# Performance work log

Hardware: AMD Instinct MI355X
Metric: run time of the kernel (lower is better)

Reference implementation:

```python
import jax, jax.numpy as jnp
import numpy as np

GRID_SIZE = 5
SPLINE_ORDER = 3
GRID_RANGE = (-1.0, 1.0)
BN_EPS = 1e-5


def _make_grid():
    h = (GRID_RANGE[1] - GRID_RANGE[0]) / GRID_SIZE
    # grid_size + 2*spline_order + 1 = 12 knots, shared across the 9 patch features
    return jnp.arange(-SPLINE_ORDER, GRID_SIZE + SPLINE_ORDER + 1, dtype=jnp.float32) * h + GRID_RANGE[0]


def _b_splines(x, grid):
    # x: (N, F) -> (N, F, grid_size + spline_order) via Cox-de Boor recursion
    x = x[..., None]
    bases = ((x >= grid[:-1]) & (x < grid[1:])).astype(x.dtype)
    for k in range(1, SPLINE_ORDER + 1):
        left = (x - grid[: -(k + 1)]) / (grid[k:-1] - grid[: -(k + 1)]) * bases[..., :-1]
        right = (grid[k + 1:] - x) / (grid[k + 1:] - grid[1:-k]) * bases[..., 1:]
        bases = left + right
    return bases


def setup_inputs() -> dict:
    key = jax.random.key(0)
    ks = jax.random.split(key, 4)
    B, C, H, W = 4, 64, 96, 96
    return {
        "x": jax.random.normal(ks[0], (B, C, H, W), dtype=jnp.float32),
        "base_weight": jax.random.normal(ks[1], (1, 9), dtype=jnp.float32) * 0.3,
        "spline_weight": jax.random.normal(ks[2], (1, 9, GRID_SIZE + SPLINE_ORDER), dtype=jnp.float32) * 0.3,
        "spline_scaler": jax.random.normal(ks[3], (1, 9), dtype=jnp.float32) * 0.3 + 1.0,
        "bn_gamma": jnp.ones((C,), dtype=jnp.float32),
        "bn_beta": jnp.zeros((C,), dtype=jnp.float32),
    }


def reference(x, base_weight, spline_weight, spline_scaler, bn_gamma, bn_beta):
    B, C, H, W = x.shape
    grid = _make_grid()
    # Per-channel depthwise 3x3 patch extraction (pad 1, stride 1), shared KANLinear(9 -> 1)
    patches = jax.lax.conv_general_dilated_patches(
        x.reshape(B * C, 1, H, W), (3, 3), (1, 1), [(1, 1), (1, 1)]
    )  # (B*C, 9, H, W)
    tok = patches.transpose(0, 2, 3, 1).reshape(-1, 9)  # (N, 9)

    base_out = jax.nn.silu(tok) @ base_weight.T  # (N, 1)
    bases = _b_splines(tok, grid)  # (N, 9, 8)
    scaled_sw = (spline_weight * spline_scaler[..., None]).reshape(1, -1)  # (1, 72)
    spline_out = bases.reshape(tok.shape[0], -1) @ scaled_sw.T  # (N, 1)

    y = (base_out + spline_out).reshape(B, C, H, W)

    # BatchNorm2d (training-mode batch statistics) + ReLU
    mean = y.mean(axis=(0, 2, 3))
    var = y.var(axis=(0, 2, 3))
    y_hat = (y - mean[None, :, None, None]) * jax.lax.rsqrt(var + BN_EPS)[None, :, None, None]
    out = jax.nn.relu(y_hat * bn_gamma[None, :, None, None] + bn_beta[None, :, None, None])
    return out
```

## Files before the change

### kernel.cpp

```cpp
#include <hip/hip_runtime.h>
#include <math.h>

#define HH 96
#define WW 96
#define CC 64
#define BB 4
#define PLANE (HH * WW)
#define NPLANES (BB * CC)
#define NPC (BB * PLANE)
#define TILE 32
#define TPL 3
#define NTILES (TPL * TPL)
#define HALO 34
#define HALO_N (HALO * HALO)
#define BLOCK 256

typedef _Float16 h2v __attribute__((ext_vector_type(2)));

static __device__ __forceinline__ float dot2h(unsigned a, unsigned b, float c) {
#if __has_builtin(__builtin_amdgcn_fdot2)
    return __builtin_amdgcn_fdot2(__builtin_bit_cast(h2v, a),
                                  __builtin_bit_cast(h2v, b), c, false);
#else
    h2v x = __builtin_bit_cast(h2v, a);
    h2v y = __builtin_bit_cast(h2v, b);
    return c + (float)x[0] * (float)y[0] + (float)x[1] * (float)y[1];
#endif
}

static __device__ __forceinline__ unsigned pk16(float a, float b) {
    return __builtin_bit_cast(unsigned, __builtin_amdgcn_cvt_pkrtz(a, b));
}


__global__ __launch_bounds__(BLOCK) void kconv_stage1(
    const float* __restrict__ x,
    const float* __restrict__ base_w,
    const float* __restrict__ spline_w,
    const float* __restrict__ spline_s,
    float* __restrict__ y,
    float2* __restrict__ part)
{
    __shared__ uint4  s_n[HALO_N];
    __shared__ float  s_sl[HALO_N];
    __shared__ unsigned s_wp[36];
    __shared__ float  s_bw[9];
    __shared__ float2 red[4];

    const int tid = threadIdx.x;

    if (tid < 36) {
        const int j = tid >> 2;
        const int k = tid & 3;
        const float sc = spline_s[j];
        s_wp[tid] = pk16(spline_w[j * 8 + 2 * k] * sc,
                         spline_w[j * 8 + 2 * k + 1] * sc);
    }
    if (tid < 9) s_bw[tid] = base_w[tid];

    const int plane = blockIdx.y;
    const int h0 = blockIdx.x * TILE;
    const float* xp = x + (size_t)plane * PLANE;

    int hy[5], hx[5];
#pragma unroll
    for (int s = 0; s < 5; ++s) {
        const int i = tid + s * BLOCK;
        const int r = i / HALO;
        hy[s] = r;
        hx[s] = i - r * HALO;
    }

    const int tx  = tid & 31;
    const int ty4 = (tid >> 5) * 4;

    for (int wt = 0; wt < TPL; ++wt) {
        const int w0 = wt * TILE;

        float v[5];
#pragma unroll
        for (int s = 0; s < 5; ++s) {
            const int gh = h0 + hy[s] - 1;
            const int gw = w0 + hx[s] - 1;
            const bool ok = (tid + s * BLOCK < HALO_N) &&
                            gh >= 0 && gh < HH && gw >= 0 && gw < WW;
            v[s] = ok ? xp[gh * WW + gw] : 0.0f;
        }

        if (wt == 0) __syncthreads();

#pragma unroll
        for (int s = 0; s < 5; ++s) {
            const int i = tid + s * BLOCK;
            if (i >= HALO_N) break;
            const float vv = v[s];
            const float e  = __expf(-vv);
            const float sl = vv * __builtin_amdgcn_rcpf(1.0f + e);

            const float sp = fmaf(vv, 2.5f, 2.5f);
            const float tf = floorf(sp);
            const float u  = sp - tf;
            const int   t  = (int)tf;
            const int   m  = t >> 1;
            const bool  odd = (t & 1) != 0;

            const float w1m = 1.0f - u;
            const float u2 = u * u;
            const float u3 = u2 * u;
            const float B0 = w1m * w1m * (w1m * (1.0f / 6.0f));
            const float B3 = u2 * (u * (1.0f / 6.0f));
            const float B1 = fmaf(-u2, 1.0f, fmaf(u3, 0.5f, 2.0f / 3.0f));
            const float B2 = 1.0f - B0 - B1 - B3;

            const unsigned h01 = pk16(B0, B1);
            const unsigned h23 = pk16(B2, B3);

            unsigned n[4];
            unsigned a_prev;
            {
                const int k0 = -1 - m;
                a_prev = (k0 == 0) ? h01 : ((k0 == 1) ? h23 : 0u);
            }
#pragma unroll
            for (int d = 0; d < 4; ++d) {
                const int k0 = d - m;
                const unsigned a_cur = (k0 == 0) ? h01 : ((k0 == 1) ? h23 : 0u);
                const unsigned sh = __builtin_amdgcn_alignbit(a_cur, a_prev, 16);
                n[d] = odd ? sh : a_cur;
                a_prev = a_cur;
            }
            s_n[i]  = make_uint4(n[0], n[1], n[2], n[3]);
            s_sl[i] = sl;
        }
        __syncthreads();

        unsigned wp[36];
        float bw[9];
#pragma unroll
        for (int q = 0; q < 36; ++q)
            wp[q] = __builtin_amdgcn_readfirstlane(s_wp[q]);
#pragma unroll
        for (int q = 0; q < 9; ++q)
            bw[q] = __int_as_float(__builtin_amdgcn_readfirstlane(__float_as_int(s_bw[q])));

        float acc[4] = {0.0f, 0.0f, 0.0f, 0.0f};
#pragma unroll
        for (int r = 0; r < 6; ++r) {
            const int base = (ty4 + r) * HALO + tx;
            uint4 cn[3];
            float cs[3];
#pragma unroll
            for (int dw = 0; dw < 3; ++dw) {
                cn[dw] = s_n[base + dw];
                cs[dw] = s_sl[base + dw];
            }
#pragma unroll
            for (int k = 0; k < 4; ++k) {
                const int dh = r - k;
                if (dh >= 0 && dh < 3) {
#pragma unroll
                    for (int dw = 0; dw < 3; ++dw) {
                        const int j = dh * 3 + dw;
                        float a = acc[k];
                        a = dot2h(cn[dw].x, wp[j * 4 + 0], a);
                        a = dot2h(cn[dw].y, wp[j * 4 + 1], a);
                        a = dot2h(cn[dw].z, wp[j * 4 + 2], a);
                        a = dot2h(cn[dw].w, wp[j * 4 + 3], a);
                        a = fmaf(bw[j], cs[dw], a);
                        acc[k] = a;
                    }
                }
            }
        }

        float lsum = 0.0f, lsq = 0.0f;
        float* yp = y + (size_t)plane * PLANE + (size_t)h0 * WW + w0;
#pragma unroll
        for (int k = 0; k < 4; ++k) {
            yp[(ty4 + k) * WW + tx] = acc[k];
            lsum += acc[k];
            lsq = fmaf(acc[k], acc[k], lsq);
        }

#pragma unroll
        for (int off = 32; off; off >>= 1) {
            lsum += __shfl_down(lsum, off, 64);
            lsq  += __shfl_down(lsq,  off, 64);
        }
        if ((tid & 63) == 0) red[tid >> 6] = make_float2(lsum, lsq);
        __syncthreads();
        if (tid == 0) {
            const float s = red[0].x + red[1].x + red[2].x + red[3].x;
            const float q = red[0].y + red[1].y + red[2].y + red[3].y;
            part[plane * NTILES + blockIdx.x * TPL + wt] = make_float2(s, q);
        }
    }
}

__global__ __launch_bounds__(BLOCK) void kconv_stage2(
    float* __restrict__ y,
    const float2* __restrict__ part,
    const float* __restrict__ gamma,
    const float* __restrict__ beta)
{
    __shared__ float2 sb;
    const int tid = threadIdx.x;
    const int plane = blockIdx.x;
    const int c = plane & (CC - 1);

    if (tid < 64) {
        float s = 0.0f, q = 0.0f;
        if (tid < 36) {
            const int b = tid / 9;
            const int t = tid - b * 9;
            const float2 pp = part[(c + CC * b) * NTILES + t];
            s = pp.x; q = pp.y;
        }
#pragma unroll
        for (int off = 32; off; off >>= 1) {
            s += __shfl_down(s, off, 64);
            q += __shfl_down(q, off, 64);
        }
        if (tid == 0) {
            const float inv = 1.0f / (float)NPC;
            const float mean = s * inv;
            const float var  = q * inv - mean * mean;
            const float sc   = rsqrtf(var + 1e-5f) * gamma[c];
            sb = make_float2(sc, beta[c] - mean * sc);
        }
    }
    __syncthreads();
    const float2 sbv = sb;

    float4* yp = (float4*)(y + (size_t)plane * PLANE + (size_t)blockIdx.y * 1024);
    float4 v = yp[tid];
    v.x = fmaxf(fmaf(v.x, sbv.x, sbv.y), 0.0f);
    v.y = fmaxf(fmaf(v.y, sbv.x, sbv.y), 0.0f);
    v.z = fmaxf(fmaf(v.z, sbv.x, sbv.y), 0.0f);
    v.w = fmaxf(fmaf(v.w, sbv.x, sbv.y), 0.0f);
    yp[tid] = v;
}

extern "C" void kernel_launch(void* const* d_in, const int* in_sizes, int n_in,
                              void* d_out, int out_size, void* d_ws, size_t ws_size,
                              hipStream_t stream)
{
    const float* x        = (const float*)d_in[0];
    const float* base_w   = (const float*)d_in[1];
    const float* spline_w = (const float*)d_in[2];
    const float* spline_s = (const float*)d_in[3];
    const float* gamma    = (const float*)d_in[4];
    const float* beta     = (const float*)d_in[5];
    float* out   = (float*)d_out;
    float2* part = (float2*)d_ws;

    dim3 g1(TPL, NPLANES);
    kconv_stage1<<<g1, BLOCK, 0, stream>>>(x, base_w, spline_w, spline_s, out, part);

    dim3 g2(NPLANES, PLANE / (BLOCK * 4));
    kconv_stage2<<<g2, BLOCK, 0, stream>>>(out, part, gamma, beta);
}
```

Measured before the change: 86.23 us.

## Use 16-row strips per block with deferred stores and single stats reduction

Stage 1 now gives each block a 16x96 strip instead of a 32x96 band, so the grid doubles to 6 strips per plane and each thread computes 2 rows per tile instead of 4. Accumulators for all three column tiles are kept in registers and written out at the end, with one block reduction and one partial-stat write per strip. Weight broadcast is hoisted out of the tile loop and launch bounds request 6 blocks per SM. This raises parallelism and cuts per-tile syncs, but increases halo recomputation (18 rows per 16 outputs versus 34 per 32) and register pressure.

```diff
diff --git a/kernel.cpp b/kernel.cpp
--- a/kernel.cpp
+++ b/kernel.cpp
@@ -8,11 +8,13 @@
 #define PLANE (HH * WW)
 #define NPLANES (BB * CC)
 #define NPC (BB * PLANE)
-#define TILE 32
+#define TILE_W 32
+#define TILE_H 16
+#define STRIPS (HH / TILE_H)
 #define TPL 3
-#define NTILES (TPL * TPL)
-#define HALO 34
-#define HALO_N (HALO * HALO)
+#define HALO_W 34
+#define HALO_H 18
+#define HALO_N (HALO_H * HALO_W)
 #define BLOCK 256
 
 typedef _Float16 h2v __attribute__((ext_vector_type(2)));
@@ -33,7 +35,7 @@
 }
 
 
-__global__ __launch_bounds__(BLOCK) void kconv_stage1(
+__global__ __launch_bounds__(BLOCK, 6) void kconv_stage1(
     const float* __restrict__ x,
     const float* __restrict__ base_w,
     const float* __restrict__ spline_w,
@@ -59,27 +61,42 @@
     if (tid < 9) s_bw[tid] = base_w[tid];
 
     const int plane = blockIdx.y;
-    const int h0 = blockIdx.x * TILE;
+    const int strip = blockIdx.x;
+    const int h0 = strip * TILE_H;
     const float* xp = x + (size_t)plane * PLANE;
 
-    int hy[5], hx[5];
-#pragma unroll
-    for (int s = 0; s < 5; ++s) {
+    int hy[3], hx[3];
+#pragma unroll
+    for (int s = 0; s < 3; ++s) {
         const int i = tid + s * BLOCK;
-        const int r = i / HALO;
+        const int r = i / HALO_W;
         hy[s] = r;
-        hx[s] = i - r * HALO;
+        hx[s] = i - r * HALO_W;
     }
 
     const int tx  = tid & 31;
-    const int ty4 = (tid >> 5) * 4;
-
+    const int ty2 = (tid >> 5) * 2;
+
+    __syncthreads();
+
+    unsigned wp[36];
+    float bw[9];
+#pragma unroll
+    for (int q = 0; q < 36; ++q)
+        wp[q] = __builtin_amdgcn_readfirstlane(s_wp[q]);
+#pragma unroll
+    for (int q = 0; q < 9; ++q)
+        bw[q] = __int_as_float(__builtin_amdgcn_readfirstlane(__float_as_int(s_bw[q])));
+
+    float acc[TPL][2] = {};
+
+#pragma unroll
     for (int wt = 0; wt < TPL; ++wt) {
-        const int w0 = wt * TILE;
-
-        float v[5];
-#pragma unroll
-        for (int s = 0; s < 5; ++s) {
+        const int w0 = wt * TILE_W;
+
+        float v[3];
+#pragma unroll
+        for (int s = 0; s < 3; ++s) {
             const int gh = h0 + hy[s] - 1;
             const int gw = w0 + hx[s] - 1;
             const bool ok = (tid + s * BLOCK < HALO_N) &&
@@ -87,10 +104,10 @@
             v[s] = ok ? xp[gh * WW + gw] : 0.0f;
         }
 
-        if (wt == 0) __syncthreads();
-
-#pragma unroll
-        for (int s = 0; s < 5; ++s) {
+        if (wt) __syncthreads();
+
+#pragma unroll
+        for (int s = 0; s < 3; ++s) {
             const int i = tid + s * BLOCK;
             if (i >= HALO_N) break;
             const float vv = v[s];
@@ -134,19 +151,9 @@
         }
         __syncthreads();
 
-        unsigned wp[36];
-        float bw[9];
-#pragma unroll
-        for (int q = 0; q < 36; ++q)
-            wp[q] = __builtin_amdgcn_readfirstlane(s_wp[q]);
-#pragma unroll
-        for (int q = 0; q < 9; ++q)
-            bw[q] = __int_as_float(__builtin_amdgcn_readfirstlane(__float_as_int(s_bw[q])));
-
-        float acc[4] = {0.0f, 0.0f, 0.0f, 0.0f};
-#pragma unroll
-        for (int r = 0; r < 6; ++r) {
-            const int base = (ty4 + r) * HALO + tx;
+#pragma unroll
+        for (int r = 0; r < 4; ++r) {
+            const int base = (ty2 + r) * HALO_W + tx;
             uint4 cn[3];
             float cs[3];
 #pragma unroll
@@ -155,45 +162,49 @@
                 cs[dw] = s_sl[base + dw];
             }
 #pragma unroll
-            for (int k = 0; k < 4; ++k) {
+            for (int k = 0; k < 2; ++k) {
                 const int dh = r - k;
                 if (dh >= 0 && dh < 3) {
+                    float a = acc[wt][k];
 #pragma unroll
                     for (int dw = 0; dw < 3; ++dw) {
                         const int j = dh * 3 + dw;
-                        float a = acc[k];
                         a = dot2h(cn[dw].x, wp[j * 4 + 0], a);
                         a = dot2h(cn[dw].y, wp[j * 4 + 1], a);
                         a = dot2h(cn[dw].z, wp[j * 4 + 2], a);
                         a = dot2h(cn[dw].w, wp[j * 4 + 3], a);
                         a = fmaf(bw[j], cs[dw], a);
-                        acc[k] = a;
                     }
+                    acc[wt][k] = a;
                 }
             }
         }
-
-        float lsum = 0.0f, lsq = 0.0f;
-        float* yp = y + (size_t)plane * PLANE + (size_t)h0 * WW + w0;
-#pragma unroll
-        for (int k = 0; k < 4; ++k) {
-            yp[(ty4 + k) * WW + tx] = acc[k];
-            lsum += acc[k];
-            lsq = fmaf(acc[k], acc[k], lsq);
-        }
-
-#pragma unroll
-        for (int off = 32; off; off >>= 1) {
-            lsum += __shfl_down(lsum, off, 64);
-            lsq  += __shfl_down(lsq,  off, 64);
-        }
-        if ((tid & 63) == 0) red[tid >> 6] = make_float2(lsum, lsq);
-        __syncthreads();
-        if (tid == 0) {
-            const float s = red[0].x + red[1].x + red[2].x + red[3].x;
-            const float q = red[0].y + red[1].y + red[2].y + red[3].y;
-            part[plane * NTILES + blockIdx.x * TPL + wt] = make_float2(s, q);
-        }
+    }
+
+    float lsum = 0.0f, lsq = 0.0f;
+    float* ypl = y + (size_t)plane * PLANE + (size_t)h0 * WW;
+#pragma unroll
+    for (int wt = 0; wt < TPL; ++wt) {
+#pragma unroll
+        for (int k = 0; k < 2; ++k) {
+            const float a = acc[wt][k];
+            ypl[(ty2 + k) * WW + wt * TILE_W + tx] = a;
+            lsum += a;
+            lsq = fmaf(a, a, lsq);
+        }
+    }
+
+#pragma unroll
+    for (int off = 32; off; off >>= 1) {
+        lsum += __shfl_down(lsum, off, 64);
+        lsq  += __shfl_down(lsq,  off, 64);
+    }
+    if ((tid & 63) == 0) red[tid >> 6] = make_float2(lsum, lsq);
+    __syncthreads();
+    if (tid == 0) {
+        const float s = red[0].x + red[1].x + red[2].x + red[3].x;
+        const float q = red[0].y + red[1].y + red[2].y + red[3].y;
+        part[plane * STRIPS + strip] = make_float2(s, q);
     }
 }
 
@@ -210,10 +221,10 @@
 
     if (tid < 64) {
         float s = 0.0f, q = 0.0f;
-        if (tid < 36) {
-            const int b = tid / 9;
-            const int t = tid - b * 9;
-            const float2 pp = part[(c + CC * b) * NTILES + t];
+        if (tid < BB * STRIPS) {
+            const int b = tid / STRIPS;
+            const int t = tid - b * STRIPS;
+            const float2 pp = part[(c + CC * b) * STRIPS + t];
             s = pp.x; q = pp.y;
         }
 #pragma unroll
@@ -254,7 +265,7 @@
     float* out   = (float*)d_out;
     float2* part = (float2*)d_ws;
 
-    dim3 g1(TPL, NPLANES);
+    dim3 g1(STRIPS, NPLANES);
     kconv_stage1<<<g1, BLOCK, 0, stream>>>(x, base_w, spline_w, spline_s, out, part);
 
     dim3 g2(NPLANES, PLANE / (BLOCK * 4));
```

Result: slower. 127.9 us (+48.3%).

## Fuse BatchNorm into conv kernel via cooperative grid sync, keeping outputs in registers

Applied to the files above, without the earlier changes.

Makes each block hold accumulators for all three width tiles in registers, and reduces the per-block partial sums to one (sum, sumsq) pair per block. The kernel launches cooperatively, synchronizes the whole grid, then applies BN and ReLU directly from registers. This drops the second kernel launch and the global write/read round trip of y. The cost is higher register pressure and a grid-wide barrier over 768 blocks that must all be resident at once. If the cooperative launch fails, it falls back to the two-kernel path.

```diff
diff --git a/kernel.cpp b/kernel.cpp
--- a/kernel.cpp
+++ b/kernel.cpp
@@ -1,5 +1,8 @@
 #include <hip/hip_runtime.h>
+#include <hip/hip_cooperative_groups.h>
 #include <math.h>
+
+namespace cg = cooperative_groups;
 
 #define HH 96
 #define WW 96
@@ -10,7 +13,6 @@
 #define NPC (BB * PLANE)
 #define TILE 32
 #define TPL 3
-#define NTILES (TPL * TPL)
 #define HALO 34
 #define HALO_N (HALO * HALO)
 #define BLOCK 256
@@ -33,11 +35,14 @@
 }
 
 
-__global__ __launch_bounds__(BLOCK) void kconv_stage1(
+template <int COOP>
+__global__ __launch_bounds__(BLOCK) void kconv_main(
     const float* __restrict__ x,
     const float* __restrict__ base_w,
     const float* __restrict__ spline_w,
     const float* __restrict__ spline_s,
+    const float* __restrict__ gamma,
+    const float* __restrict__ beta,
     float* __restrict__ y,
     float2* __restrict__ part)
 {
@@ -46,6 +51,7 @@
     __shared__ unsigned s_wp[36];
     __shared__ float  s_bw[9];
     __shared__ float2 red[4];
+    __shared__ float2 sb;
 
     const int tid = threadIdx.x;
 
@@ -59,6 +65,8 @@
     if (tid < 9) s_bw[tid] = base_w[tid];
 
     const int plane = blockIdx.y;
+    const int c = plane & (CC - 1);
+    const int b = plane >> 6;
     const int h0 = blockIdx.x * TILE;
     const float* xp = x + (size_t)plane * PLANE;
 
@@ -73,6 +81,11 @@
 
     const int tx  = tid & 31;
     const int ty4 = (tid >> 5) * 4;
+
+    float acc[TPL][4] = {};
+
+    unsigned wp[36];
+    float bw[9];
 
     for (int wt = 0; wt < TPL; ++wt) {
         const int w0 = wt * TILE;
@@ -87,7 +100,16 @@
             v[s] = ok ? xp[gh * WW + gw] : 0.0f;
         }
 
-        if (wt == 0) __syncthreads();
+        __syncthreads();
+
+        if (wt == 0) {
+#pragma unroll
+            for (int q = 0; q < 36; ++q)
+                wp[q] = __builtin_amdgcn_readfirstlane(s_wp[q]);
+#pragma unroll
+            for (int q = 0; q < 9; ++q)
+                bw[q] = __int_as_float(__builtin_amdgcn_readfirstlane(__float_as_int(s_bw[q])));
+        }
 
 #pragma unroll
         for (int s = 0; s < 5; ++s) {
@@ -134,16 +156,6 @@
         }
         __syncthreads();
 
-        unsigned wp[36];
-        float bw[9];
-#pragma unroll
-        for (int q = 0; q < 36; ++q)
-            wp[q] = __builtin_amdgcn_readfirstlane(s_wp[q]);
-#pragma unroll
-        for (int q = 0; q < 9; ++q)
-            bw[q] = __int_as_float(__builtin_amdgcn_readfirstlane(__float_as_int(s_bw[q])));
-
-        float acc[4] = {0.0f, 0.0f, 0.0f, 0.0f};
 #pragma unroll
         for (int r = 0; r < 6; ++r) {
             const int base = (ty4 + r) * HALO + tx;
@@ -158,46 +170,87 @@
             for (int k = 0; k < 4; ++k) {
                 const int dh = r - k;
                 if (dh >= 0 && dh < 3) {
+                    float a = acc[wt][k];
 #pragma unroll
                     for (int dw = 0; dw < 3; ++dw) {
                         const int j = dh * 3 + dw;
-                        float a = acc[k];
                         a = dot2h(cn[dw].x, wp[j * 4 + 0], a);
                         a = dot2h(cn[dw].y, wp[j * 4 + 1], a);
                         a = dot2h(cn[dw].z, wp[j * 4 + 2], a);
                         a = dot2h(cn[dw].w, wp[j * 4 + 3], a);
                         a = fmaf(bw[j], cs[dw], a);
-                        acc[k] = a;
                     }
+                    acc[wt][k] = a;
                 }
             }
         }
-
-        float lsum = 0.0f, lsq = 0.0f;
-        float* yp = y + (size_t)plane * PLANE + (size_t)h0 * WW + w0;
+    }
+
+    float lsum = 0.0f, lsq = 0.0f;
+#pragma unroll
+    for (int wt = 0; wt < TPL; ++wt)
 #pragma unroll
         for (int k = 0; k < 4; ++k) {
-            yp[(ty4 + k) * WW + tx] = acc[k];
-            lsum += acc[k];
-            lsq = fmaf(acc[k], acc[k], lsq);
-        }
-
-#pragma unroll
-        for (int off = 32; off; off >>= 1) {
-            lsum += __shfl_down(lsum, off, 64);
-            lsq  += __shfl_down(lsq,  off, 64);
-        }
-        if ((tid & 63) == 0) red[tid >> 6] = make_float2(lsum, lsq);
+            lsum += acc[wt][k];
+            lsq = fmaf(acc[wt][k], acc[wt][k], lsq);
+        }
+#pragma unroll
+    for (int off = 32; off; off >>= 1) {
+        lsum += __shfl_down(lsum, off, 64);
+        lsq  += __shfl_down(lsq,  off, 64);
+    }
+    if ((tid & 63) == 0) red[tid >> 6] = make_float2(lsum, lsq);
+    __syncthreads();
+    if (tid == 0) {
+        const float s = red[0].x + red[1].x + red[2].x + red[3].x;
+        const float q = red[0].y + red[1].y + red[2].y + red[3].y;
+        part[c * 12 + b * 3 + blockIdx.x] = make_float2(s, q);
+    }
+
+    if (COOP) {
+        cg::this_grid().sync();
+
+        if (tid < 64) {
+            float s = 0.0f, q = 0.0f;
+            if (tid < 12) {
+                const float2 pp = part[c * 12 + tid];
+                s = pp.x; q = pp.y;
+            }
+#pragma unroll
+            for (int off = 8; off; off >>= 1) {
+                s += __shfl_down(s, off, 64);
+                q += __shfl_down(q, off, 64);
+            }
+            if (tid == 0) {
+                const float inv = 1.0f / (float)NPC;
+                const float mean = s * inv;
+                const float var  = q * inv - mean * mean;
+                const float scl  = rsqrtf(var + 1e-5f) * gamma[c];
+                sb = make_float2(scl, beta[c] - mean * scl);
+            }
+        }
         __syncthreads();
-        if (tid == 0) {
-            const float s = red[0].x + red[1].x + red[2].x + red[3].x;
-            const float q = red[0].y + red[1].y + red[2].y + red[3].y;
-            part[plane * NTILES + blockIdx.x * TPL + wt] = make_float2(s, q);
-        }
-    }
-}
-
-__global__ __launch_bounds__(BLOCK) void kconv_stage2(
+        const float2 sbv = sb;
+
+        float* ypl = y + (size_t)plane * PLANE + (size_t)h0 * WW;
+#pragma unroll
+        for (int wt = 0; wt < TPL; ++wt)
+#pragma unroll
+            for (int k = 0; k < 4; ++k) {
+                const float o = fmaxf(fmaf(acc[wt][k], sbv.x, sbv.y), 0.0f);
+                ypl[(ty4 + k) * WW + wt * TILE + tx] = o;
+            }
+    } else {
+        float* ypl = y + (size_t)plane * PLANE + (size_t)h0 * WW;
+#pragma unroll
+        for (int wt = 0; wt < TPL; ++wt)
+#pragma unroll
+            for (int k = 0; k < 4; ++k)
+                ypl[(ty4 + k) * WW + wt * TILE + tx] = acc[wt][k];
+    }
+}
+
+__global__ __launch_bounds__(BLOCK) void kconv_bn(
     float* __restrict__ y,
     const float2* __restrict__ part,
     const float* __restrict__ gamma,
@@ -210,14 +263,12 @@
 
     if (tid < 64) {
         float s = 0.0f, q = 0.0f;
-        if (tid < 36) {
-            const int b = tid / 9;
-            const int t = tid - b * 9;
-            const float2 pp = part[(c + CC * b) * NTILES + t];
+        if (tid < 12) {
+            const float2 pp = part[c * 12 + tid];
             s = pp.x; q = pp.y;
         }
 #pragma unroll
-        for (int off = 32; off; off >>= 1) {
+        for (int off = 8; off; off >>= 1) {
             s += __shfl_down(s, off, 64);
             q += __shfl_down(q, off, 64);
         }
@@ -254,9 +305,18 @@
     float* out   = (float*)d_out;
     float2* part = (float2*)d_ws;
 
-    dim3 g1(TPL, NPLANES);
-    kconv_stage1<<<g1, BLOCK, 0, stream>>>(x, base_w, spline_w, spline_s, out, part);
-
-    dim3 g2(NPLANES, PLANE / (BLOCK * 4));
-    kconv_stage2<<<g2, BLOCK, 0, stream>>>(out, part, gamma, beta);
-}
+    void* kargs[] = {(void*)&x, (void*)&base_w, (void*)&spline_w, (void*)&spline_s,
+                     (void*)&gamma, (void*)&beta, (void*)&out, (void*)&part};
+    dim3 g(TPL, NPLANES);
+
+    hipError_t err = hipLaunchCooperativeKernel(
+        (const void*)(kconv_main<1>), g, dim3(BLOCK), kargs, 0, stream);
+
+    if (err != hipSuccess) {
+        (void)hipGetLastError();
+        kconv_main<0><<<g, BLOCK, 0, stream>>>(x, base_w, spline_w, spline_s,
+                                               gamma, beta, out, part);
+        dim3 g2(NPLANES, PLANE / (BLOCK * 4));
+        kconv_bn<<<g2, BLOCK, 0, stream>>>(out, part, gamma, beta);
+    }
+}
```

Result: slower. 150.3 us (+74.4%).

## Double-buffer halo tiles in LDS and accumulate BN stats per block

Applied to the files above, without the earlier changes.

Stage 1 now keeps two LDS buffers. While the current tile is being convolved, it loads and preprocesses the next column tile's halo (SiLU and B-spline packing), which is meant to overlap global loads with compute and cut the per-tile barriers. BN partial sums are accumulated across the three tiles and written once per block, so stage 2 reduces 12 partials instead of 36. Doubled LDS use (about 44KB) may lower occupancy. The per-dh accumulator is also kept in a register across dw.

```diff
diff --git a/kernel.cpp b/kernel.cpp
--- a/kernel.cpp
+++ b/kernel.cpp
@@ -41,8 +41,8 @@
     float* __restrict__ y,
     float2* __restrict__ part)
 {
-    __shared__ uint4  s_n[HALO_N];
-    __shared__ float  s_sl[HALO_N];
+    __shared__ uint4  s_n[2][HALO_N];
+    __shared__ float  s_sl[2][HALO_N];
     __shared__ unsigned s_wp[36];
     __shared__ float  s_bw[9];
     __shared__ float2 red[4];
@@ -74,74 +74,83 @@
     const int tx  = tid & 31;
     const int ty4 = (tid >> 5) * 4;
 
+    float lsum = 0.0f, lsq = 0.0f;
+
+    float v[5];
+#pragma unroll
+    for (int s = 0; s < 5; ++s) {
+        const int gh = h0 + hy[s] - 1;
+        const int gw = hx[s] - 1;
+        const bool ok = (tid + s * BLOCK < HALO_N) &&
+                        gh >= 0 && gh < HH && gw >= 0 && gw < WW;
+        v[s] = ok ? xp[gh * WW + gw] : 0.0f;
+    }
+#pragma unroll
+    for (int s = 0; s < 5; ++s) {
+        const int i = tid + s * BLOCK;
+        if (i >= HALO_N) break;
+        const float vv = v[s];
+        const float e  = __expf(-vv);
+        const float sl = vv * __builtin_amdgcn_rcpf(1.0f + e);
+        const float sp = fmaf(vv, 2.5f, 2.5f);
+        const float tf = floorf(sp);
+        const float u  = sp - tf;
+        const int   t  = (int)tf;
+        const int   m  = t >> 1;
+        const bool  odd = (t & 1) != 0;
+        const float w1m = 1.0f - u;
+        const float u2 = u * u;
+        const float u3 = u2 * u;
+        const float B0 = w1m * w1m * (w1m * (1.0f / 6.0f));
+        const float B3 = u2 * (u * (1.0f / 6.0f));
+        const float B1 = fmaf(-u2, 1.0f, fmaf(u3, 0.5f, 2.0f / 3.0f));
+        const float B2 = 1.0f - B0 - B1 - B3;
+        const unsigned h01 = pk16(B0, B1);
+        const unsigned h23 = pk16(B2, B3);
+        unsigned n[4];
+        unsigned a_prev;
+        {
+            const int k0 = -1 - m;
+            a_prev = (k0 == 0) ? h01 : ((k0 == 1) ? h23 : 0u);
+        }
+#pragma unroll
+        for (int d = 0; d < 4; ++d) {
+            const int k0 = d - m;
+            const unsigned a_cur = (k0 == 0) ? h01 : ((k0 == 1) ? h23 : 0u);
+            const unsigned sh = __builtin_amdgcn_alignbit(a_cur, a_prev, 16);
+            n[d] = odd ? sh : a_cur;
+            a_prev = a_cur;
+        }
+        s_n[0][i]  = make_uint4(n[0], n[1], n[2], n[3]);
+        s_sl[0][i] = sl;
+    }
+    __syncthreads();
+
+    unsigned wp[36];
+    float bw[9];
+#pragma unroll
+    for (int q = 0; q < 36; ++q)
+        wp[q] = __builtin_amdgcn_readfirstlane(s_wp[q]);
+#pragma unroll
+    for (int q = 0; q < 9; ++q)
+        bw[q] = __int_as_float(__builtin_amdgcn_readfirstlane(__float_as_int(s_bw[q])));
+
+#pragma unroll
     for (int wt = 0; wt < TPL; ++wt) {
-        const int w0 = wt * TILE;
-
-        float v[5];
-#pragma unroll
-        for (int s = 0; s < 5; ++s) {
-            const int gh = h0 + hy[s] - 1;
-            const int gw = w0 + hx[s] - 1;
-            const bool ok = (tid + s * BLOCK < HALO_N) &&
-                            gh >= 0 && gh < HH && gw >= 0 && gw < WW;
-            v[s] = ok ? xp[gh * WW + gw] : 0.0f;
-        }
-
-        if (wt == 0) __syncthreads();
-
-#pragma unroll
-        for (int s = 0; s < 5; ++s) {
-            const int i = tid + s * BLOCK;
-            if (i >= HALO_N) break;
-            const float vv = v[s];
-            const float e  = __expf(-vv);
-            const float sl = vv * __builtin_amdgcn_rcpf(1.0f + e);
-
-            const float sp = fmaf(vv, 2.5f, 2.5f);
-            const float tf = floorf(sp);
-            const float u  = sp - tf;
-            const int   t  = (int)tf;
-            const int   m  = t >> 1;
-            const bool  odd = (t & 1) != 0;
-
-            const float w1m = 1.0f - u;
-            const float u2 = u * u;
-            const float u3 = u2 * u;
-            const float B0 = w1m * w1m * (w1m * (1.0f / 6.0f));
-            const float B3 = u2 * (u * (1.0f / 6.0f));
-            const float B1 = fmaf(-u2, 1.0f, fmaf(u3, 0.5f, 2.0f / 3.0f));
-            const float B2 = 1.0f - B0 - B1 - B3;
-
-            const unsigned h01 = pk16(B0, B1);
-            const unsigned h23 = pk16(B2, B3);
-
-            unsigned n[4];
-            unsigned a_prev;
-            {
-                const int k0 = -1 - m;
-                a_prev = (k0 == 0) ? h01 : ((k0 == 1) ? h23 : 0u);
+        const int cur = wt & 1;
+        const int nxt = cur ^ 1;
+
+        if (wt < TPL - 1) {
+            const int w0n = (wt + 1) * TILE;
+#pragma unroll
+            for (int s = 0; s < 5; ++s) {
+                const int gh = h0 + hy[s] - 1;
+                const int gw = w0n + hx[s] - 1;
+                const bool ok = (tid + s * BLOCK < HALO_N) &&
+                                gh >= 0 && gh < HH && gw >= 0 && gw < WW;
+                v[s] = ok ? xp[gh * WW + gw] : 0.0f;
             }
-#pragma unroll
-            for (int d = 0; d < 4; ++d) {
-                const int k0 = d - m;
-                const unsigned a_cur = (k0 == 0) ? h01 : ((k0 == 1) ? h23 : 0u);
-                const unsigned sh = __builtin_amdgcn_alignbit(a_cur, a_prev, 16);
-                n[d] = odd ? sh : a_cur;
-                a_prev = a_cur;
-            }
-            s_n[i]  = make_uint4(n[0], n[1], n[2], n[3]);
-            s_sl[i] = sl;
-        }
-        __syncthreads();
-
-        unsigned wp[36];
-        float bw[9];
-#pragma unroll
-        for (int q = 0; q < 36; ++q)
-            wp[q] = __builtin_amdgcn_readfirstlane(s_wp[q]);
-#pragma unroll
-        for (int q = 0; q < 9; ++q)
-            bw[q] = __int_as_float(__builtin_amdgcn_readfirstlane(__float_as_int(s_bw[q])));
+        }
 
         float acc[4] = {0.0f, 0.0f, 0.0f, 0.0f};
 #pragma unroll
@@ -151,30 +160,29 @@
             float cs[3];
 #pragma unroll
             for (int dw = 0; dw < 3; ++dw) {
-                cn[dw] = s_n[base + dw];
-                cs[dw] = s_sl[base + dw];
+                cn[dw] = s_n[cur][base + dw];
+                cs[dw] = s_sl[cur][base + dw];
             }
 #pragma unroll
             for (int k = 0; k < 4; ++k) {
                 const int dh = r - k;
                 if (dh >= 0 && dh < 3) {
+                    float a = acc[k];
 #pragma unroll
                     for (int dw = 0; dw < 3; ++dw) {
                         const int j = dh * 3 + dw;
-                        float a = acc[k];
                         a = dot2h(cn[dw].x, wp[j * 4 + 0], a);
                         a = dot2h(cn[dw].y, wp[j * 4 + 1], a);
                         a = dot2h(cn[dw].z, wp[j * 4 + 2], a);
                         a = dot2h(cn[dw].w, wp[j * 4 + 3], a);
                         a = fmaf(bw[j], cs[dw], a);
-                        acc[k] = a;
                     }
+                    acc[k] = a;
                 }
             }
         }
 
-        float lsum = 0.0f, lsq = 0.0f;
-        float* yp = y + (size_t)plane * PLANE + (size_t)h0 * WW + w0;
+        float* yp = y + (size_t)plane * PLANE + (size_t)h0 * WW + wt * TILE;
 #pragma unroll
         for (int k = 0; k < 4; ++k) {
             yp[(ty4 + k) * WW + tx] = acc[k];
@@ -182,18 +190,61 @@
             lsq = fmaf(acc[k], acc[k], lsq);
         }
 
-#pragma unroll
-        for (int off = 32; off; off >>= 1) {
-            lsum += __shfl_down(lsum, off, 64);
-            lsq  += __shfl_down(lsq,  off, 64);
-        }
-        if ((tid & 63) == 0) red[tid >> 6] = make_float2(lsum, lsq);
-        __syncthreads();
-        if (tid == 0) {
-            const float s = red[0].x + red[1].x + red[2].x + red[3].x;
-            const float q = red[0].y + red[1].y + red[2].y + red[3].y;
-            part[plane * NTILES + blockIdx.x * TPL + wt] = make_float2(s, q);
-        }
+        if (wt < TPL - 1) {
+#pragma unroll
+            for (int s = 0; s < 5; ++s) {
+                const int i = tid + s * BLOCK;
+                if (i >= HALO_N) break;
+                const float vv = v[s];
+                const float e  = __expf(-vv);
+                const float sl = vv * __builtin_amdgcn_rcpf(1.0f + e);
+                const float sp = fmaf(vv, 2.5f, 2.5f);
+                const float tf = floorf(sp);
+                const float u  = sp - tf;
+                const int   t  = (int)tf;
+                const int   m  = t >> 1;
+                const bool  odd = (t & 1) != 0;
+                const float w1m = 1.0f - u;
+                const float u2 = u * u;
+                const float u3 = u2 * u;
+                const float B0 = w1m * w1m * (w1m * (1.0f / 6.0f));
+                const float B3 = u2 * (u * (1.0f / 6.0f));
+                const float B1 = fmaf(-u2, 1.0f, fmaf(u3, 0.5f, 2.0f / 3.0f));
+                const float B2 = 1.0f - B0 - B1 - B3;
+                const unsigned h01 = pk16(B0, B1);
+                const unsigned h23 = pk16(B2, B3);
+                unsigned n[4];
+                unsigned a_prev;
+                {
+                    const int k0 = -1 - m;
+                    a_prev = (k0 == 0) ? h01 : ((k0 == 1) ? h23 : 0u);
+                }
+#pragma unroll
+                for (int d = 0; d < 4; ++d) {
+                    const int k0 = d - m;
+                    const unsigned a_cur = (k0 == 0) ? h01 : ((k0 == 1) ? h23 : 0u);
+                    const unsigned sh = __builtin_amdgcn_alignbit(a_cur, a_prev, 16);
+                    n[d] = odd ? sh : a_cur;
+                    a_prev = a_cur;
+                }
+                s_n[nxt][i]  = make_uint4(n[0], n[1], n[2], n[3]);
+                s_sl[nxt][i] = sl;
+            }
+            __syncthreads();
+        }
+    }
+
+#pragma unroll
+    for (int off = 32; off; off >>= 1) {
+        lsum += __shfl_down(lsum, off, 64);
+        lsq  += __shfl_down(lsq,  off, 64);
+    }
+    if ((tid & 63) == 0) red[tid >> 6] = make_float2(lsum, lsq);
+    __syncthreads();
+    if (tid == 0) {
+        const float s = red[0].x + red[1].x + red[2].x + red[3].x;
+        const float q = red[0].y + red[1].y + red[2].y + red[3].y;
+        part[plane * NTILES + blockIdx.x] = make_float2(s, q);
     }
 }
 
@@ -210,14 +261,14 @@
 
     if (tid < 64) {
         float s = 0.0f, q = 0.0f;
-        if (tid < 36) {
-            const int b = tid / 9;
-            const int t = tid - b * 9;
+        if (tid < 12) {
+            const int b = tid / 3;
+            const int t = tid - b * 3;
             const float2 pp = part[(c + CC * b) * NTILES + t];
             s = pp.x; q = pp.y;
         }
 #pragma unroll
-        for (int off = 32; off; off >>= 1) {
+        for (int off = 8; off; off >>= 1) {
             s += __shfl_down(s, off, 64);
             q += __shfl_down(q, off, 64);
         }
```

Measured after the change: 85.60 us. About the same (-0.7%).
